# Performance work log

Measured on AMD Instinct MI355X. Metric: run time of the kernel, lower is better.

The kernel has to match this reference:

```python
import jax, jax.numpy as jnp
import numpy as np

N = 20000
E = 320000
IN_FEATS = 512
H = 4
D_HID = 256
D_OUT = 256
NEG_SLOPE = 0.2


def _gat_layer(h, src, dst, Wsrc, Wdst, al, ar, b, apply_act):
    # h: [N, Fin]; Wsrc/Wdst: [Fin, H*D]; al/ar: [H, D]; b: [H*D]
    Hh, Dd = al.shape
    fs = (h @ Wsrc).reshape(-1, Hh, Dd)  # [N, H, D] src projection
    fd = (h @ Wdst).reshape(-1, Hh, Dd)  # [N, H, D] dst projection
    el = (fs * al).sum(-1)               # [N, H]
    er = (fd * ar).sum(-1)               # [N, H]
    e = jax.nn.leaky_relu(el[src] + er[dst], NEG_SLOPE)  # [E, H]
    m = jax.lax.stop_gradient(jax.ops.segment_max(e, dst, num_segments=N))
    m = jnp.where(jnp.isfinite(m), m, 0.0)
    ex = jnp.exp(e - m[dst])
    den = jax.ops.segment_sum(ex, dst, num_segments=N)  # [N, H]
    alpha = ex / den[dst]                               # edge softmax per dst node
    msg = fs[src] * alpha[:, :, None]                   # [E, H, D]
    out = jax.ops.segment_sum(msg, dst, num_segments=N) + b.reshape(Hh, Dd)
    if apply_act:
        out = jax.nn.relu(out)
    return out  # [N, H, D]


def setup_inputs() -> dict:
    key = jax.random.key(0)
    ks = jax.random.split(key, 20)
    x = jax.random.normal(ks[0], (N, IN_FEATS), dtype=jnp.float32)
    src = jax.random.randint(ks[1], (E,), 0, N, dtype=jnp.int32)
    dst = jax.random.randint(ks[2], (E,), 0, N, dtype=jnp.int32)
    fins = [IN_FEATS, H * D_HID, H * D_HID]
    douts = [D_HID, D_HID, D_OUT]
    inp = {"x": x, "src": src, "dst": dst}
    ki = 3
    for l in range(3):
        fin, do = fins[l], douts[l]
        s = 1.0 / np.sqrt(fin)
        inp[f"Wsrc{l}"] = jax.random.normal(ks[ki], (fin, H * do), dtype=jnp.float32) * s; ki += 1
        inp[f"Wdst{l}"] = jax.random.normal(ks[ki], (fin, H * do), dtype=jnp.float32) * s; ki += 1
        inp[f"al{l}"] = jax.random.normal(ks[ki], (H, do), dtype=jnp.float32) * 0.1; ki += 1
        inp[f"ar{l}"] = jax.random.normal(ks[ki], (H, do), dtype=jnp.float32) * 0.1; ki += 1
        inp[f"b{l}"] = jnp.zeros((H * do,), dtype=jnp.float32)
    return inp


def reference(x, src, dst,
              Wsrc0, Wdst0, al0, ar0, b0,
              Wsrc1, Wdst1, al1, ar1, b1,
              Wsrc2, Wdst2, al2, ar2, b2):
    h = _gat_layer(x, src, dst, Wsrc0, Wdst0, al0, ar0, b0, True).reshape(N, -1)
    h = _gat_layer(h, src, dst, Wsrc1, Wdst1, al1, ar1, b1, True).reshape(N, -1)
    h = _gat_layer(h, src, dst, Wsrc2, Wdst2, al2, ar2, b2, False)  # [N, H, D_OUT]
    return h.mean(axis=1)  # [N, D_OUT]
```

## Files before the change

### kernel.cpp

```cpp
#include <hip/hip_runtime.h>
#include <hip/hip_bf16.h>
#include <math.h>

#define NNODES 20000
#define NPAD   20480
#define NBM    160
#define NEDGES 320000
#define HEADS  4
#define DDIM   256
#define MCOLS  1024

typedef __attribute__((ext_vector_type(8))) short short8;
typedef __attribute__((ext_vector_type(4))) float f32x4;

__device__ __forceinline__ unsigned short f2bf(float f) {
  unsigned u = __float_as_uint(f);
  unsigned r = (u + 0x7fffu + ((u >> 16) & 1u)) >> 16;
  return (unsigned short)r;
}
__device__ __forceinline__ float bf2f(unsigned short h) {
  return __uint_as_float(((unsigned)h) << 16);
}
__device__ __forceinline__ float blo(unsigned v) { return __uint_as_float(v << 16); }
__device__ __forceinline__ float bhi(unsigned v) { return __uint_as_float(v & 0xffff0000u); }

__device__ __forceinline__ void async_ld16(void* lds, const void* g) {
  __builtin_amdgcn_global_load_lds(
      (const __attribute__((address_space(1))) unsigned int*)g,
      (__attribute__((address_space(3))) unsigned int*)lds, 16, 0, 0);
}

__global__ void k_zero(int* deg, int n) {
  int i = blockIdx.x*blockDim.x + threadIdx.x;
  if (i < n) deg[i] = 0;
}
__global__ void k_hist(const int* __restrict__ dst, int* deg, int e) {
  int i = blockIdx.x*blockDim.x + threadIdx.x;
  if (i < e) atomicAdd(&deg[dst[i]], 1);
}
__global__ void k_scan(const int* __restrict__ deg, int* row_ptr, int* cursor) {
  __shared__ int sm[1024];
  int t = threadIdx.x;
  const int CH = 20;
  int base = t*CH;
  int s = 0;
  #pragma unroll
  for (int i = 0; i < CH; ++i) { int idx = base+i; if (idx < NNODES) s += deg[idx]; }
  int val = s;
  sm[t] = s; __syncthreads();
  for (int off = 1; off < 1024; off <<= 1) {
    int add = (t >= off) ? sm[t-off] : 0;
    __syncthreads();
    val += add; sm[t] = val;
    __syncthreads();
  }
  int run = val - s;
  for (int i = 0; i < CH; ++i) {
    int idx = base+i;
    if (idx < NNODES) { row_ptr[idx] = run; cursor[idx] = run; run += deg[idx]; }
  }
  if (t == 0) row_ptr[NNODES] = NEDGES;
}
__global__ void k_fill(const int* __restrict__ src, const int* __restrict__ dst,
                       int* cursor, int* srcs_sorted, int* dsts_sorted, int e) {
  int i = blockIdx.x*blockDim.x + threadIdx.x;
  if (i < e) {
    int d = dst[i];
    int pos = atomicAdd(&cursor[d], 1);
    srcs_sorted[pos] = src[i];
    dsts_sorted[pos] = d;
  }
}

__device__ __forceinline__ void fold_body(const float* __restrict__ W,
                                          const float* __restrict__ v,
                                          float* __restrict__ F, int K, int bb) {
  int wave = threadIdx.x >> 6, lane = threadIdx.x & 63;
  int p = bb*4 + wave;
  int k = p >> 2, h = p & 3;
  const float4 wv = *(const float4*)&W[(size_t)k*MCOLS + h*DDIM + lane*4];
  const float4 av = *(const float4*)&v[h*DDIM + lane*4];
  float s = wv.x*av.x + wv.y*av.y + wv.z*av.z + wv.w*av.w;
  for (int off = 32; off; off >>= 1) s += __shfl_xor(s, off);
  if (lane == 0) F[k*HEADS + h] = s;
}
__global__ __launch_bounds__(256) void k_fold_all(
    const float* Wd0, const float* ar0, float* F0,
    const float* Ws0, const float* al0, float* G0,
    const float* Wd1, const float* ar1, float* F1,
    const float* Ws1, const float* al1, float* G1,
    const float* Wd2, const float* ar2, float* F2,
    const float* Ws2, const float* al2, float* G2) {
  int b = blockIdx.x;
  if      (b < 512)  fold_body(Wd0, ar0, F0, 512,  b);
  else if (b < 1024) fold_body(Ws0, al0, G0, 512,  b - 512);
  else if (b < 2048) fold_body(Wd1, ar1, F1, 1024, b - 1024);
  else if (b < 3072) fold_body(Ws1, al1, G1, 1024, b - 2048);
  else if (b < 4096) fold_body(Wd2, ar2, F2, 1024, b - 3072);
  else               fold_body(Ws2, al2, G2, 1024, b - 4096);
}

__global__ __launch_bounds__(256) void k_prep0(
    const float* __restrict__ x, const float* __restrict__ Wal,
    const float* __restrict__ Wred,
    unsigned short* __restrict__ hi, unsigned short* __restrict__ lo,
    float* __restrict__ el, float* __restrict__ er) {
  __shared__ float red_sm[4][8];
  int n = blockIdx.x, t = threadIdx.x;
  if (n >= NNODES) {
    *(ushort2*)&hi[(size_t)n*512 + 2*t] = (ushort2){0,0};
    *(ushort2*)&lo[(size_t)n*512 + 2*t] = (ushort2){0,0};
    return;
  }
  float2 xv = *(const float2*)&x[(size_t)n*512 + 2*t];
  ushort2 h2, l2;
  h2.x = f2bf(xv.x); l2.x = f2bf(xv.x - bf2f(h2.x));
  h2.y = f2bf(xv.y); l2.y = f2bf(xv.y - bf2f(h2.y));
  *(ushort2*)&hi[(size_t)n*512 + 2*t] = h2;
  *(ushort2*)&lo[(size_t)n*512 + 2*t] = l2;
  const float4 wa0 = *(const float4*)&Wal[(2*t)*4];
  const float4 wa1 = *(const float4*)&Wal[(2*t+1)*4];
  const float4 wr0 = *(const float4*)&Wred[(2*t)*4];
  const float4 wr1 = *(const float4*)&Wred[(2*t+1)*4];
  float p[8];
  p[0] = xv.x*wa0.x + xv.y*wa1.x;
  p[1] = xv.x*wa0.y + xv.y*wa1.y;
  p[2] = xv.x*wa0.z + xv.y*wa1.z;
  p[3] = xv.x*wa0.w + xv.y*wa1.w;
  p[4] = xv.x*wr0.x + xv.y*wr1.x;
  p[5] = xv.x*wr0.y + xv.y*wr1.y;
  p[6] = xv.x*wr0.z + xv.y*wr1.z;
  p[7] = xv.x*wr0.w + xv.y*wr1.w;
  for (int off = 32; off; off >>= 1)
    #pragma unroll
    for (int j = 0; j < 8; ++j) p[j] += __shfl_xor(p[j], off);
  if ((t & 63) == 0)
    #pragma unroll
    for (int j = 0; j < 8; ++j) red_sm[t >> 6][j] = p[j];
  __syncthreads();
  if (t < 8) {
    float v = (red_sm[0][t] + red_sm[1][t]) + (red_sm[2][t] + red_sm[3][t]);
    if (t < 4) el[n*HEADS + t] = v;
    else       er[n*HEADS + (t-4)] = v;
  }
}

__global__ __launch_bounds__(256) void k_cvtw_wgt(
    const float* __restrict__ W, unsigned short* __restrict__ Th, int K,
    const float* __restrict__ el, const float* __restrict__ er,
    const int* __restrict__ srcs, const int* __restrict__ dsts,
    float* __restrict__ wb, int e4) {
  int b = blockIdx.x;
  if (b < K) {
    __shared__ float sm[32][33];
    int n0 = (b & 31)*32, k0 = (b >> 5)*32;
    int t = threadIdx.x;
    int r = t >> 3, c4 = (t & 7)*4;
    *(float4*)&sm[r][c4] = *(const float4*)&W[(size_t)(k0 + r)*MCOLS + n0 + c4];
    __syncthreads();
    ushort4 h;
    h.x = f2bf(sm[c4+0][r]);
    h.y = f2bf(sm[c4+1][r]);
    h.z = f2bf(sm[c4+2][r]);
    h.w = f2bf(sm[c4+3][r]);
    *(ushort4*)&Th[(size_t)(n0 + r)*K + k0 + c4] = h;
  } else {
    int i = (b - K)*256 + threadIdx.x;
    if (i < e4) {
      int pos = i >> 2, h = i & 3;
      float v = el[srcs[pos]*HEADS + h] + er[dsts[pos]*HEADS + h];
      v = v >= 0.f ? v : 0.2f*v;
      wb[i] = __expf(v);
    }
  }
}

template<bool SPLIT>
__global__ __launch_bounds__(256, 3) void k_gemm_mfma(
    const unsigned short* __restrict__ Ah, const unsigned short* __restrict__ Al,
    const unsigned short* __restrict__ Bh,
    unsigned short* __restrict__ Fh, int K) {
  __shared__ short sAh[128*32];
  __shared__ short sAl[SPLIT ? 128*32 : 16];
  __shared__ short sBh[128*32];
  const int t = threadIdx.x;
  const int w = t >> 6, l = t & 63;
  const int b = blockIdx.x;
  const int xcd = b & 7, kk = b >> 3;
  const int bm = xcd*20 + (kk >> 3), bn = kk & 7;
  const int m0 = (w >> 1) * 64, n0 = (w & 1) * 64;

  f32x4 acc[4][4];
  #pragma unroll
  for (int i = 0; i < 4; ++i)
    #pragma unroll
    for (int j = 0; j < 4; ++j) acc[i][j] = (f32x4){0.f, 0.f, 0.f, 0.f};

  const int srow = t >> 2, koct = (t & 3) * 8;
  const size_t r64 = (size_t)64 * K;
  const unsigned short* gAh = Ah + (size_t)(bm*128 + srow)*K + koct;
  const unsigned short* gAl = Al + (size_t)(bm*128 + srow)*K + koct;
  const unsigned short* gBh = Bh + (size_t)(bn*128 + srow)*K + koct;
  char* lAh = (char*)sAh + w*1024;
  char* lAl = (char*)sAl + w*1024;
  char* lBh = (char*)sBh + w*1024;

  const int fr = l & 15, fq = l >> 4;

  for (int k0 = 0; k0 < K; k0 += 32) {
    async_ld16(lAh,        gAh + k0);
    async_ld16(lAh + 4096, gAh + k0 + r64);
    if (SPLIT) {
      async_ld16(lAl,        gAl + k0);
      async_ld16(lAl + 4096, gAl + k0 + r64);
    }
    async_ld16(lBh,        gBh + k0);
    async_ld16(lBh + 4096, gBh + k0 + r64);
    __syncthreads();

    short8 bhv[4];
    #pragma unroll
    for (int nt = 0; nt < 4; ++nt)
      bhv[nt] = *(const short8*)&sBh[(n0 + nt*16 + fr)*32 + fq*8];
    #pragma unroll
    for (int mt = 0; mt < 4; ++mt) {
      int off = (m0 + mt*16 + fr)*32 + fq*8;
      short8 ah = *(const short8*)&sAh[off];
      #pragma unroll
      for (int nt = 0; nt < 4; ++nt)
        acc[mt][nt] = __builtin_amdgcn_mfma_f32_16x16x32_bf16(ah, bhv[nt], acc[mt][nt], 0, 0, 0);
      if (SPLIT) {
        short8 al = *(const short8*)&sAl[off];
        #pragma unroll
        for (int nt = 0; nt < 4; ++nt)
          acc[mt][nt] = __builtin_amdgcn_mfma_f32_16x16x32_bf16(al, bhv[nt], acc[mt][nt], 0, 0, 0);
      }
    }
    __syncthreads();
  }

  #pragma unroll
  for (int mt = 0; mt < 4; ++mt)
    #pragma unroll
    for (int nt = 0; nt < 4; ++nt) {
      size_t base = (size_t)(bm*128 + m0 + mt*16 + fq*4)*MCOLS + bn*128 + n0 + nt*16 + fr;
      Fh[base          ] = f2bf(acc[mt][nt][0]);
      Fh[base + MCOLS  ] = f2bf(acc[mt][nt][1]);
      Fh[base + 2*MCOLS] = f2bf(acc[mt][nt][2]);
      Fh[base + 3*MCOLS] = f2bf(acc[mt][nt][3]);
    }
}

__global__ __launch_bounds__(128) void k_agg_f(
    const unsigned short* __restrict__ fsh, const float* __restrict__ wbuf,
    const int* __restrict__ row_ptr, const int* __restrict__ srcs,
    const float* __restrict__ bias,
    const float* __restrict__ WalN, const float* __restrict__ WredN,
    unsigned short* __restrict__ Ahi,
    float* __restrict__ el_next, float* __restrict__ er_next) {
  __shared__ float red_sm[2][8];
  int n = blockIdx.x;
  int t = threadIdx.x;
  int w = t >> 6, lane = t & 63;
  int half = lane >> 5, lam = lane & 31;
  int head = w*2 + half;
  int k0 = head*DDIM + lam*8;
  if (n >= NNODES) {
    uint4 z = {0,0,0,0};
    *(uint4*)&Ahi[(size_t)n*MCOLS + k0] = z;
    return;
  }
  int beg = row_ptr[n], end = row_ptr[n+1];
  float den = 0.f;
  float ac[8];
  #pragma unroll
  for (int j = 0; j < 8; ++j) ac[j] = 0.f;
  const char* fbyte = (const char*)fsh;
  const unsigned tb = (unsigned)(k0*2);

  int nfull = (end - beg) & ~7;
  int gend = beg + nfull;
  int i = beg;
  int s[8];
  if (i < gend) {
    #pragma unroll
    for (int j = 0; j < 8; ++j) s[j] = srcs[i + j];
  }
  while (i < gend) {
    float wg[8];
    #pragma unroll
    for (int j = 0; j < 8; ++j) {
      float2 wv = *(const float2*)&wbuf[(size_t)(i + j)*HEADS + w*2];
      wg[j] = half ? wv.y : wv.x;
    }
    uint4 u[8];
    #pragma unroll
    for (int j = 0; j < 8; ++j)
      u[j] = *(const uint4*)(fbyte + ((unsigned)s[j]*2048u + tb));
    i += 8;
    if (i < gend) {
      #pragma unroll
      for (int j = 0; j < 8; ++j) s[j] = srcs[i + j];
    }
    #pragma unroll
    for (int j = 0; j < 8; ++j) {
      den += wg[j];
      ac[0] = fmaf(wg[j], blo(u[j].x), ac[0]);
      ac[1] = fmaf(wg[j], bhi(u[j].x), ac[1]);
      ac[2] = fmaf(wg[j], blo(u[j].y), ac[2]);
      ac[3] = fmaf(wg[j], bhi(u[j].y), ac[3]);
      ac[4] = fmaf(wg[j], blo(u[j].z), ac[4]);
      ac[5] = fmaf(wg[j], bhi(u[j].z), ac[5]);
      ac[6] = fmaf(wg[j], blo(u[j].w), ac[6]);
      ac[7] = fmaf(wg[j], bhi(u[j].w), ac[7]);
    }
  }
  for (; i < end; ++i) {
    int sr = srcs[i];
    float2 wv = *(const float2*)&wbuf[(size_t)i*HEADS + w*2];
    float wgt = half ? wv.y : wv.x;
    const uint4 u = *(const uint4*)(fbyte + ((unsigned)sr*2048u + tb));
    den += wgt;
    ac[0] = fmaf(wgt, blo(u.x), ac[0]);
    ac[1] = fmaf(wgt, bhi(u.x), ac[1]);
    ac[2] = fmaf(wgt, blo(u.y), ac[2]);
    ac[3] = fmaf(wgt, bhi(u.y), ac[3]);
    ac[4] = fmaf(wgt, blo(u.z), ac[4]);
    ac[5] = fmaf(wgt, bhi(u.z), ac[5]);
    ac[6] = fmaf(wgt, blo(u.w), ac[6]);
    ac[7] = fmaf(wgt, bhi(u.w), ac[7]);
  }
  float inv = den > 0.f ? 1.f/den : 0.f;
  const float4 bv0 = *(const float4*)&bias[k0];
  const float4 bv1 = *(const float4*)&bias[k0 + 4];
  float o[8];
  o[0] = fmaxf(ac[0]*inv + bv0.x, 0.f);
  o[1] = fmaxf(ac[1]*inv + bv0.y, 0.f);
  o[2] = fmaxf(ac[2]*inv + bv0.z, 0.f);
  o[3] = fmaxf(ac[3]*inv + bv0.w, 0.f);
  o[4] = fmaxf(ac[4]*inv + bv1.x, 0.f);
  o[5] = fmaxf(ac[5]*inv + bv1.y, 0.f);
  o[6] = fmaxf(ac[6]*inv + bv1.z, 0.f);
  o[7] = fmaxf(ac[7]*inv + bv1.w, 0.f);
  uint4 hp;
  hp.x = (unsigned)f2bf(o[0]) | ((unsigned)f2bf(o[1]) << 16);
  hp.y = (unsigned)f2bf(o[2]) | ((unsigned)f2bf(o[3]) << 16);
  hp.z = (unsigned)f2bf(o[4]) | ((unsigned)f2bf(o[5]) << 16);
  hp.w = (unsigned)f2bf(o[6]) | ((unsigned)f2bf(o[7]) << 16);
  *(uint4*)&Ahi[(size_t)n*MCOLS + k0] = hp;
  float p[8];
  #pragma unroll
  for (int j = 0; j < 8; ++j) p[j] = 0.f;
  #pragma unroll
  for (int j = 0; j < 8; ++j) {
    const float4 wa = *(const float4*)&WalN[(k0+j)*HEADS];
    const float4 wr = *(const float4*)&WredN[(k0+j)*HEADS];
    p[0] = fmaf(o[j], wa.x, p[0]);
    p[1] = fmaf(o[j], wa.y, p[1]);
    p[2] = fmaf(o[j], wa.z, p[2]);
    p[3] = fmaf(o[j], wa.w, p[3]);
    p[4] = fmaf(o[j], wr.x, p[4]);
    p[5] = fmaf(o[j], wr.y, p[5]);
    p[6] = fmaf(o[j], wr.z, p[6]);
    p[7] = fmaf(o[j], wr.w, p[7]);
  }
  for (int off = 32; off; off >>= 1)
    #pragma unroll
    for (int j = 0; j < 8; ++j) p[j] += __shfl_xor(p[j], off);
  if (lane == 0)
    #pragma unroll
    for (int j = 0; j < 8; ++j) red_sm[w][j] = p[j];
  __syncthreads();
  if (t < 8) {
    float v = red_sm[0][t] + red_sm[1][t];
    if (t < 4) el_next[n*HEADS + t] = v;
    else       er_next[n*HEADS + (t-4)] = v;
  }
}

__global__ __launch_bounds__(128) void k_agg_out(
    const unsigned short* __restrict__ fsh, const float* __restrict__ wbuf,
    const int* __restrict__ row_ptr, const int* __restrict__ srcs,
    const float* __restrict__ bias, float* __restrict__ out) {
  __shared__ float sm[HEADS*DDIM];
  int n = blockIdx.x;
  int t = threadIdx.x;
  int w = t >> 6, lane = t & 63;
  int half = lane >> 5, lam = lane & 31;
  int head = w*2 + half;
  int k0 = head*DDIM + lam*8;
  int beg = row_ptr[n], end = row_ptr[n+1];
  float den = 0.f;
  float ac[8];
  #pragma unroll
  for (int j = 0; j < 8; ++j) ac[j] = 0.f;
  const char* fbyte = (const char*)fsh;
  const unsigned tb = (unsigned)(k0*2);

  int nfull = (end - beg) & ~7;
  int gend = beg + nfull;
  int i = beg;
  int s[8];
  if (i < gend) {
    #pragma unroll
    for (int j = 0; j < 8; ++j) s[j] = srcs[i + j];
  }
  while (i < gend) {
    float wg[8];
    #pragma unroll
    for (int j = 0; j < 8; ++j) {
      float2 wv = *(const float2*)&wbuf[(size_t)(i + j)*HEADS + w*2];
      wg[j] = half ? wv.y : wv.x;
    }
    uint4 u[8];
    #pragma unroll
    for (int j = 0; j < 8; ++j)
      u[j] = *(const uint4*)(fbyte + ((unsigned)s[j]*2048u + tb));
    i += 8;
    if (i < gend) {
      #pragma unroll
      for (int j = 0; j < 8; ++j) s[j] = srcs[i + j];
    }
    #pragma unroll
    for (int j = 0; j < 8; ++j) {
      den += wg[j];
      ac[0] = fmaf(wg[j], blo(u[j].x), ac[0]);
      ac[1] = fmaf(wg[j], bhi(u[j].x), ac[1]);
      ac[2] = fmaf(wg[j], blo(u[j].y), ac[2]);
      ac[3] = fmaf(wg[j], bhi(u[j].y), ac[3]);
      ac[4] = fmaf(wg[j], blo(u[j].z), ac[4]);
      ac[5] = fmaf(wg[j], bhi(u[j].z), ac[5]);
      ac[6] = fmaf(wg[j], blo(u[j].w), ac[6]);
      ac[7] = fmaf(wg[j], bhi(u[j].w), ac[7]);
    }
  }
  for (; i < end; ++i) {
    int sr = srcs[i];
    float2 wv = *(const float2*)&wbuf[(size_t)i*HEADS + w*2];
    float wgt = half ? wv.y : wv.x;
    const uint4 u = *(const uint4*)(fbyte + ((unsigned)sr*2048u + tb));
    den += wgt;
    ac[0] = fmaf(wgt, blo(u.x), ac[0]);
    ac[1] = fmaf(wgt, bhi(u.x), ac[1]);
    ac[2] = fmaf(wgt, blo(u.y), ac[2]);
    ac[3] = fmaf(wgt, bhi(u.y), ac[3]);
    ac[4] = fmaf(wgt, blo(u.z), ac[4]);
    ac[5] = fmaf(wgt, bhi(u.z), ac[5]);
    ac[6] = fmaf(wgt, blo(u.w), ac[6]);
    ac[7] = fmaf(wgt, bhi(u.w), ac[7]);
  }
  float inv = den > 0.f ? 1.f/den : 0.f;
  const float4 bv0 = *(const float4*)&bias[k0];
  const float4 bv1 = *(const float4*)&bias[k0 + 4];
  sm[k0+0] = ac[0]*inv + bv0.x;
  sm[k0+1] = ac[1]*inv + bv0.y;
  sm[k0+2] = ac[2]*inv + bv0.z;
  sm[k0+3] = ac[3]*inv + bv0.w;
  sm[k0+4] = ac[4]*inv + bv1.x;
  sm[k0+5] = ac[5]*inv + bv1.y;
  sm[k0+6] = ac[6]*inv + bv1.z;
  sm[k0+7] = ac[7]*inv + bv1.w;
  __syncthreads();
  #pragma unroll
  for (int rep = 0; rep < 2; ++rep) {
    int d = t + rep*128;
    out[(size_t)n*DDIM + d] =
        0.25f*((sm[d] + sm[DDIM + d]) + (sm[2*DDIM + d] + sm[3*DDIM + d]));
  }
}

extern "C" void kernel_launch(void* const* d_in, const int* in_sizes, int n_in,
                              void* d_out, int out_size, void* d_ws, size_t ws_size,
                              hipStream_t stream) {
  const float* x   = (const float*)d_in[0];
  const int*   src = (const int*)d_in[1];
  const int*   dst = (const int*)d_in[2];
  const float* Wsrc[3] = {(const float*)d_in[3], (const float*)d_in[8],  (const float*)d_in[13]};
  const float* Wdst[3] = {(const float*)d_in[4], (const float*)d_in[9],  (const float*)d_in[14]};
  const float* al[3]   = {(const float*)d_in[5], (const float*)d_in[10], (const float*)d_in[15]};
  const float* ar[3]   = {(const float*)d_in[6], (const float*)d_in[11], (const float*)d_in[16]};
  const float* bb[3]   = {(const float*)d_in[7], (const float*)d_in[12], (const float*)d_in[17]};

  char* ws = (char*)d_ws;
  size_t off = 0;
  auto alloc = [&](size_t bytes) { void* p = ws + off; off += (bytes + 255) & ~255ull; return p; };
  unsigned short* fshB = (unsigned short*)alloc((size_t)NPAD*MCOLS*2);
  unsigned short* Ahi = (unsigned short*)alloc((size_t)NPAD*MCOLS*2);
  unsigned short* Alo = (unsigned short*)alloc((size_t)NPAD*MCOLS*2);
  unsigned short* Wth = (unsigned short*)alloc((size_t)MCOLS*MCOLS*2);
  float* elA  = (float*)alloc((size_t)NNODES*HEADS*4);
  float* elB  = (float*)alloc((size_t)NNODES*HEADS*4);
  float* erA  = (float*)alloc((size_t)NNODES*HEADS*4);
  float* erB  = (float*)alloc((size_t)NNODES*HEADS*4);
  float* wbuf = (float*)alloc((size_t)NEDGES*HEADS*4);
  float* WredB[3]; float* WalB[3];
  for (int l = 0; l < 3; ++l) {
    WredB[l] = (float*)alloc(1024*HEADS*4);
    WalB[l]  = (float*)alloc(1024*HEADS*4);
  }
  int* deg     = (int*)alloc((size_t)NNODES*4);
  int* row_ptr = (int*)alloc((size_t)(NNODES+1)*4);
  int* cursor  = (int*)alloc((size_t)NNODES*4);
  int* srcs    = (int*)alloc((size_t)NEDGES*4);
  int* dsts    = (int*)alloc((size_t)NEDGES*4);
  (void)ws_size; (void)in_sizes; (void)n_in; (void)out_size;

  k_zero<<<(NNODES+255)/256, 256, 0, stream>>>(deg, NNODES);
  k_hist<<<(NEDGES+255)/256, 256, 0, stream>>>(dst, deg, NEDGES);
  k_scan<<<1, 1024, 0, stream>>>(deg, row_ptr, cursor);
  k_fill<<<(NEDGES+255)/256, 256, 0, stream>>>(src, dst, cursor, srcs, dsts, NEDGES);

  k_fold_all<<<5120, 256, 0, stream>>>(
      Wdst[0], ar[0], WredB[0], Wsrc[0], al[0], WalB[0],
      Wdst[1], ar[1], WredB[1], Wsrc[1], al[1], WalB[1],
      Wdst[2], ar[2], WredB[2], Wsrc[2], al[2], WalB[2]);

  k_prep0<<<NPAD, 256, 0, stream>>>(x, WalB[0], WredB[0], Ahi, Alo, elA, erA);

  float* el_cur = elA; float* el_nxt = elB;
  float* er_cur = erA; float* er_nxt = erB;
  const int Fin[3] = {512, 1024, 1024};
  const int E4 = NEDGES*HEADS;
  for (int l = 0; l < 3; ++l) {
    int K = Fin[l];
    k_cvtw_wgt<<<K + (E4 + 255)/256, 256, 0, stream>>>(
        Wsrc[l], Wth, K, el_cur, er_cur, srcs, dsts, wbuf, E4);
    if (l == 0)
      k_gemm_mfma<true><<<NBM*8, 256, 0, stream>>>(Ahi, Alo, Wth, fshB, K);
    else
      k_gemm_mfma<false><<<NBM*8, 256, 0, stream>>>(Ahi, Alo, Wth, fshB, K);
    if (l < 2) {
      k_agg_f<<<NPAD, 128, 0, stream>>>(fshB, wbuf, row_ptr, srcs, bb[l],
                                        WalB[l+1], WredB[l+1], Ahi, el_nxt, er_nxt);
      float* t1 = el_cur; el_cur = el_nxt; el_nxt = t1;
      float* t2 = er_cur; er_cur = er_nxt; er_nxt = t2;
    } else {
      k_agg_out<<<NNODES, 128, 0, stream>>>(fshB, wbuf, row_ptr, srcs, bb[l],
                                            (float*)d_out);
    }
  }
}
```

Before: 732.5 us.

## Split aggregation into per-slice blocks with two-phase source-range gather for L2 locality

Aggregation kernels now give each block one of 8 feature slices of 128 channels and several nodes per wave. Each wave's 4 lane groups gather edges in parallel, and each gather runs two passes over halves of the source-node range so the gathered rows stay within a smaller working set in cache. Edge weights are stored head-major so per-head reads are contiguous. Partial el/er projections are summed with atomics into buffers zeroed by memsets, and the final layer writes per-head partials that a new combine kernel averages. In exchange, every edge list is read twice, and the code adds atomics, extra launches and cross-lane shuffle reductions.

```diff
diff --git a/kernel.cpp b/kernel.cpp
--- a/kernel.cpp
+++ b/kernel.cpp
@@ -167,7 +167,8 @@
   } else {
     int i = (b - K)*256 + threadIdx.x;
     if (i < e4) {
-      int pos = i >> 2, h = i & 3;
+      int h = i / NEDGES;
+      int pos = i - h*NEDGES;
       float v = el[srcs[pos]*HEADS + h] + er[dsts[pos]*HEADS + h];
       v = v >= 0.f ? v : 0.2f*v;
       wb[i] = __expf(v);
@@ -251,222 +252,190 @@
     }
 }
 
-__global__ __launch_bounds__(128) void k_agg_f(
+__device__ __forceinline__ void slice_gather(
+    const char* __restrict__ fb, const float* __restrict__ wbh,
+    const int* __restrict__ srcs, int beg, int end, unsigned soff, int g,
+    float* ac, float& den) {
+  #pragma unroll
+  for (int ph = 0; ph < 2; ++ph) {
+    const int lo = ph * (NNODES/2);
+    const int hi = lo + (NNODES/2);
+    int e = beg + g;
+    int sr0 = 0; float wg0 = 0.f;
+    if (e < end) {
+      int sr = srcs[e];
+      float wv = wbh[e];
+      bool inr = (sr >= lo) & (sr < hi);
+      sr0 = inr ? sr : 0;
+      wg0 = inr ? wv : 0.f;
+    }
+    for (int i = beg; i < end; i += 4) {
+      const uint4 u = *(const uint4*)(fb + ((unsigned)sr0*2048u + soff));
+      int e2 = i + 4 + g;
+      int sr1 = 0; float wg1 = 0.f;
+      if (e2 < end) {
+        int sr = srcs[e2];
+        float wv = wbh[e2];
+        bool inr = (sr >= lo) & (sr < hi);
+        sr1 = inr ? sr : 0;
+        wg1 = inr ? wv : 0.f;
+      }
+      den += wg0;
+      ac[0] = fmaf(wg0, blo(u.x), ac[0]);
+      ac[1] = fmaf(wg0, bhi(u.x), ac[1]);
+      ac[2] = fmaf(wg0, blo(u.y), ac[2]);
+      ac[3] = fmaf(wg0, bhi(u.y), ac[3]);
+      ac[4] = fmaf(wg0, blo(u.z), ac[4]);
+      ac[5] = fmaf(wg0, bhi(u.z), ac[5]);
+      ac[6] = fmaf(wg0, blo(u.w), ac[6]);
+      ac[7] = fmaf(wg0, bhi(u.w), ac[7]);
+      sr0 = sr1; wg0 = wg1;
+    }
+  }
+}
+
+__global__ __launch_bounds__(256) void k_agg_f(
     const unsigned short* __restrict__ fsh, const float* __restrict__ wbuf,
     const int* __restrict__ row_ptr, const int* __restrict__ srcs,
     const float* __restrict__ bias,
     const float* __restrict__ WalN, const float* __restrict__ WredN,
     unsigned short* __restrict__ Ahi,
     float* __restrict__ el_next, float* __restrict__ er_next) {
-  __shared__ float red_sm[2][8];
-  int n = blockIdx.x;
-  int t = threadIdx.x;
-  int w = t >> 6, lane = t & 63;
-  int half = lane >> 5, lam = lane & 31;
-  int head = w*2 + half;
-  int k0 = head*DDIM + lam*8;
-  if (n >= NNODES) {
-    uint4 z = {0,0,0,0};
-    *(uint4*)&Ahi[(size_t)n*MCOLS + k0] = z;
-    return;
-  }
-  int beg = row_ptr[n], end = row_ptr[n+1];
-  float den = 0.f;
-  float ac[8];
-  #pragma unroll
-  for (int j = 0; j < 8; ++j) ac[j] = 0.f;
-  const char* fbyte = (const char*)fsh;
-  const unsigned tb = (unsigned)(k0*2);
-
-  int nfull = (end - beg) & ~7;
-  int gend = beg + nfull;
-  int i = beg;
-  int s[8];
-  if (i < gend) {
-    #pragma unroll
-    for (int j = 0; j < 8; ++j) s[j] = srcs[i + j];
-  }
-  while (i < gend) {
-    float wg[8];
+  const int b = blockIdx.x;
+  const int s = b & 7;
+  const int gb = b >> 3;
+  const int t = threadIdx.x;
+  const int wv = t >> 6, lane = t & 63;
+  const int g = lane >> 4, sl = lane & 15;
+  const int head = s >> 1, half = s & 1;
+  const int k0 = head*DDIM + half*128 + sl*8;
+  const unsigned soff = (unsigned)(s*256 + sl*16);
+  const char* fb = (const char*)fsh;
+  const float* wbh = wbuf + (size_t)head*NEDGES;
+
+  const int nbase = gb*20 + wv*5;
+  for (int nn = 0; nn < 5; ++nn) {
+    const int n = nbase + nn;
+    if (n >= NNODES) {
+      if (lane < 16) {
+        uint4 z = {0,0,0,0};
+        *(uint4*)&Ahi[(size_t)n*MCOLS + k0] = z;
+      }
+      continue;
+    }
+    const int beg = row_ptr[n], end = row_ptr[n+1];
+    float den = 0.f;
+    float ac[8] = {0.f,0.f,0.f,0.f,0.f,0.f,0.f,0.f};
+    slice_gather(fb, wbh, srcs, beg, end, soff, g, ac, den);
     #pragma unroll
     for (int j = 0; j < 8; ++j) {
-      float2 wv = *(const float2*)&wbuf[(size_t)(i + j)*HEADS + w*2];
-      wg[j] = half ? wv.y : wv.x;
-    }
-    uint4 u[8];
-    #pragma unroll
-    for (int j = 0; j < 8; ++j)
-      u[j] = *(const uint4*)(fbyte + ((unsigned)s[j]*2048u + tb));
-    i += 8;
-    if (i < gend) {
+      ac[j] += __shfl_xor(ac[j], 16);
+      ac[j] += __shfl_xor(ac[j], 32);
+    }
+    den += __shfl_xor(den, 16);
+    den += __shfl_xor(den, 32);
+    const float inv = den > 0.f ? 1.f/den : 0.f;
+    const float4 bv0 = *(const float4*)&bias[k0];
+    const float4 bv1 = *(const float4*)&bias[k0 + 4];
+    float o[8];
+    o[0] = fmaxf(ac[0]*inv + bv0.x, 0.f);
+    o[1] = fmaxf(ac[1]*inv + bv0.y, 0.f);
+    o[2] = fmaxf(ac[2]*inv + bv0.z, 0.f);
+    o[3] = fmaxf(ac[3]*inv + bv0.w, 0.f);
+    o[4] = fmaxf(ac[4]*inv + bv1.x, 0.f);
+    o[5] = fmaxf(ac[5]*inv + bv1.y, 0.f);
+    o[6] = fmaxf(ac[6]*inv + bv1.z, 0.f);
+    o[7] = fmaxf(ac[7]*inv + bv1.w, 0.f);
+    if (lane < 16) {
+      uint4 hp;
+      hp.x = (unsigned)f2bf(o[0]) | ((unsigned)f2bf(o[1]) << 16);
+      hp.y = (unsigned)f2bf(o[2]) | ((unsigned)f2bf(o[3]) << 16);
+      hp.z = (unsigned)f2bf(o[4]) | ((unsigned)f2bf(o[5]) << 16);
+      hp.w = (unsigned)f2bf(o[6]) | ((unsigned)f2bf(o[7]) << 16);
+      *(uint4*)&Ahi[(size_t)n*MCOLS + k0] = hp;
+    }
+    float p[8] = {0.f,0.f,0.f,0.f,0.f,0.f,0.f,0.f};
+    #pragma unroll
+    for (int j = 0; j < 8; ++j) {
+      const float4 wa = *(const float4*)&WalN[(k0+j)*HEADS];
+      const float4 wr = *(const float4*)&WredN[(k0+j)*HEADS];
+      p[0] = fmaf(o[j], wa.x, p[0]);
+      p[1] = fmaf(o[j], wa.y, p[1]);
+      p[2] = fmaf(o[j], wa.z, p[2]);
+      p[3] = fmaf(o[j], wa.w, p[3]);
+      p[4] = fmaf(o[j], wr.x, p[4]);
+      p[5] = fmaf(o[j], wr.y, p[5]);
+      p[6] = fmaf(o[j], wr.z, p[6]);
+      p[7] = fmaf(o[j], wr.w, p[7]);
+    }
+    #pragma unroll
+    for (int off2 = 1; off2 < 16; off2 <<= 1)
       #pragma unroll
-      for (int j = 0; j < 8; ++j) s[j] = srcs[i + j];
-    }
-    #pragma unroll
-    for (int j = 0; j < 8; ++j) {
-      den += wg[j];
-      ac[0] = fmaf(wg[j], blo(u[j].x), ac[0]);
-      ac[1] = fmaf(wg[j], bhi(u[j].x), ac[1]);
-      ac[2] = fmaf(wg[j], blo(u[j].y), ac[2]);
-      ac[3] = fmaf(wg[j], bhi(u[j].y), ac[3]);
-      ac[4] = fmaf(wg[j], blo(u[j].z), ac[4]);
-      ac[5] = fmaf(wg[j], bhi(u[j].z), ac[5]);
-      ac[6] = fmaf(wg[j], blo(u[j].w), ac[6]);
-      ac[7] = fmaf(wg[j], bhi(u[j].w), ac[7]);
-    }
-  }
-  for (; i < end; ++i) {
-    int sr = srcs[i];
-    float2 wv = *(const float2*)&wbuf[(size_t)i*HEADS + w*2];
-    float wgt = half ? wv.y : wv.x;
-    const uint4 u = *(const uint4*)(fbyte + ((unsigned)sr*2048u + tb));
-    den += wgt;
-    ac[0] = fmaf(wgt, blo(u.x), ac[0]);
-    ac[1] = fmaf(wgt, bhi(u.x), ac[1]);
-    ac[2] = fmaf(wgt, blo(u.y), ac[2]);
-    ac[3] = fmaf(wgt, bhi(u.y), ac[3]);
-    ac[4] = fmaf(wgt, blo(u.z), ac[4]);
-    ac[5] = fmaf(wgt, bhi(u.z), ac[5]);
-    ac[6] = fmaf(wgt, blo(u.w), ac[6]);
-    ac[7] = fmaf(wgt, bhi(u.w), ac[7]);
-  }
-  float inv = den > 0.f ? 1.f/den : 0.f;
-  const float4 bv0 = *(const float4*)&bias[k0];
-  const float4 bv1 = *(const float4*)&bias[k0 + 4];
-  float o[8];
-  o[0] = fmaxf(ac[0]*inv + bv0.x, 0.f);
-  o[1] = fmaxf(ac[1]*inv + bv0.y, 0.f);
-  o[2] = fmaxf(ac[2]*inv + bv0.z, 0.f);
-  o[3] = fmaxf(ac[3]*inv + bv0.w, 0.f);
-  o[4] = fmaxf(ac[4]*inv + bv1.x, 0.f);
-  o[5] = fmaxf(ac[5]*inv + bv1.y, 0.f);
-  o[6] = fmaxf(ac[6]*inv + bv1.z, 0.f);
-  o[7] = fmaxf(ac[7]*inv + bv1.w, 0.f);
-  uint4 hp;
-  hp.x = (unsigned)f2bf(o[0]) | ((unsigned)f2bf(o[1]) << 16);
-  hp.y = (unsigned)f2bf(o[2]) | ((unsigned)f2bf(o[3]) << 16);
-  hp.z = (unsigned)f2bf(o[4]) | ((unsigned)f2bf(o[5]) << 16);
-  hp.w = (unsigned)f2bf(o[6]) | ((unsigned)f2bf(o[7]) << 16);
-  *(uint4*)&Ahi[(size_t)n*MCOLS + k0] = hp;
-  float p[8];
-  #pragma unroll
-  for (int j = 0; j < 8; ++j) p[j] = 0.f;
-  #pragma unroll
-  for (int j = 0; j < 8; ++j) {
-    const float4 wa = *(const float4*)&WalN[(k0+j)*HEADS];
-    const float4 wr = *(const float4*)&WredN[(k0+j)*HEADS];
-    p[0] = fmaf(o[j], wa.x, p[0]);
-    p[1] = fmaf(o[j], wa.y, p[1]);
-    p[2] = fmaf(o[j], wa.z, p[2]);
-    p[3] = fmaf(o[j], wa.w, p[3]);
-    p[4] = fmaf(o[j], wr.x, p[4]);
-    p[5] = fmaf(o[j], wr.y, p[5]);
-    p[6] = fmaf(o[j], wr.z, p[6]);
-    p[7] = fmaf(o[j], wr.w, p[7]);
-  }
-  for (int off = 32; off; off >>= 1)
-    #pragma unroll
-    for (int j = 0; j < 8; ++j) p[j] += __shfl_xor(p[j], off);
-  if (lane == 0)
-    #pragma unroll
-    for (int j = 0; j < 8; ++j) red_sm[w][j] = p[j];
-  __syncthreads();
-  if (t < 8) {
-    float v = red_sm[0][t] + red_sm[1][t];
-    if (t < 4) el_next[n*HEADS + t] = v;
-    else       er_next[n*HEADS + (t-4)] = v;
-  }
-}
-
-__global__ __launch_bounds__(128) void k_agg_out(
+      for (int j = 0; j < 8; ++j) p[j] += __shfl_xor(p[j], off2);
+    if (lane == 0) {
+      #pragma unroll
+      for (int j = 0; j < 4; ++j) atomicAdd(&el_next[n*HEADS + j], p[j]);
+      #pragma unroll
+      for (int j = 0; j < 4; ++j) atomicAdd(&er_next[n*HEADS + j], p[4+j]);
+    }
+  }
+}
+
+__global__ __launch_bounds__(256) void k_agg_out(
     const unsigned short* __restrict__ fsh, const float* __restrict__ wbuf,
     const int* __restrict__ row_ptr, const int* __restrict__ srcs,
-    const float* __restrict__ bias, float* __restrict__ out) {
-  __shared__ float sm[HEADS*DDIM];
-  int n = blockIdx.x;
-  int t = threadIdx.x;
-  int w = t >> 6, lane = t & 63;
-  int half = lane >> 5, lam = lane & 31;
-  int head = w*2 + half;
-  int k0 = head*DDIM + lam*8;
-  int beg = row_ptr[n], end = row_ptr[n+1];
-  float den = 0.f;
-  float ac[8];
-  #pragma unroll
-  for (int j = 0; j < 8; ++j) ac[j] = 0.f;
-  const char* fbyte = (const char*)fsh;
-  const unsigned tb = (unsigned)(k0*2);
-
-  int nfull = (end - beg) & ~7;
-  int gend = beg + nfull;
-  int i = beg;
-  int s[8];
-  if (i < gend) {
-    #pragma unroll
-    for (int j = 0; j < 8; ++j) s[j] = srcs[i + j];
-  }
-  while (i < gend) {
-    float wg[8];
+    const float* __restrict__ bias, float* __restrict__ opart) {
+  const int b = blockIdx.x;
+  const int s = b & 7;
+  const int gb = b >> 3;
+  const int t = threadIdx.x;
+  const int wv = t >> 6, lane = t & 63;
+  const int g = lane >> 4, sl = lane & 15;
+  const int head = s >> 1, half = s & 1;
+  const int k0 = head*DDIM + half*128 + sl*8;
+  const unsigned soff = (unsigned)(s*256 + sl*16);
+  const char* fb = (const char*)fsh;
+  const float* wbh = wbuf + (size_t)head*NEDGES;
+
+  const int nbase = gb*20 + wv*5;
+  for (int nn = 0; nn < 5; ++nn) {
+    const int n = nbase + nn;
+    const int beg = row_ptr[n], end = row_ptr[n+1];
+    float den = 0.f;
+    float ac[8] = {0.f,0.f,0.f,0.f,0.f,0.f,0.f,0.f};
+    slice_gather(fb, wbh, srcs, beg, end, soff, g, ac, den);
     #pragma unroll
     for (int j = 0; j < 8; ++j) {
-      float2 wv = *(const float2*)&wbuf[(size_t)(i + j)*HEADS + w*2];
-      wg[j] = half ? wv.y : wv.x;
-    }
-    uint4 u[8];
-    #pragma unroll
-    for (int j = 0; j < 8; ++j)
-      u[j] = *(const uint4*)(fbyte + ((unsigned)s[j]*2048u + tb));
-    i += 8;
-    if (i < gend) {
-      #pragma unroll
-      for (int j = 0; j < 8; ++j) s[j] = srcs[i + j];
-    }
-    #pragma unroll
-    for (int j = 0; j < 8; ++j) {
-      den += wg[j];
-      ac[0] = fmaf(wg[j], blo(u[j].x), ac[0]);
-      ac[1] = fmaf(wg[j], bhi(u[j].x), ac[1]);
-      ac[2] = fmaf(wg[j], blo(u[j].y), ac[2]);
-      ac[3] = fmaf(wg[j], bhi(u[j].y), ac[3]);
-      ac[4] = fmaf(wg[j], blo(u[j].z), ac[4]);
-      ac[5] = fmaf(wg[j], bhi(u[j].z), ac[5]);
-      ac[6] = fmaf(wg[j], blo(u[j].w), ac[6]);
-      ac[7] = fmaf(wg[j], bhi(u[j].w), ac[7]);
-    }
-  }
-  for (; i < end; ++i) {
-    int sr = srcs[i];
-    float2 wv = *(const float2*)&wbuf[(size_t)i*HEADS + w*2];
-    float wgt = half ? wv.y : wv.x;
-    const uint4 u = *(const uint4*)(fbyte + ((unsigned)sr*2048u + tb));
-    den += wgt;
-    ac[0] = fmaf(wgt, blo(u.x), ac[0]);
-    ac[1] = fmaf(wgt, bhi(u.x), ac[1]);
-    ac[2] = fmaf(wgt, blo(u.y), ac[2]);
-    ac[3] = fmaf(wgt, bhi(u.y), ac[3]);
-    ac[4] = fmaf(wgt, blo(u.z), ac[4]);
-    ac[5] = fmaf(wgt, bhi(u.z), ac[5]);
-    ac[6] = fmaf(wgt, blo(u.w), ac[6]);
-    ac[7] = fmaf(wgt, bhi(u.w), ac[7]);
-  }
-  float inv = den > 0.f ? 1.f/den : 0.f;
-  const float4 bv0 = *(const float4*)&bias[k0];
-  const float4 bv1 = *(const float4*)&bias[k0 + 4];
-  sm[k0+0] = ac[0]*inv + bv0.x;
-  sm[k0+1] = ac[1]*inv + bv0.y;
-  sm[k0+2] = ac[2]*inv + bv0.z;
-  sm[k0+3] = ac[3]*inv + bv0.w;
-  sm[k0+4] = ac[4]*inv + bv1.x;
-  sm[k0+5] = ac[5]*inv + bv1.y;
-  sm[k0+6] = ac[6]*inv + bv1.z;
-  sm[k0+7] = ac[7]*inv + bv1.w;
-  __syncthreads();
-  #pragma unroll
-  for (int rep = 0; rep < 2; ++rep) {
-    int d = t + rep*128;
-    out[(size_t)n*DDIM + d] =
-        0.25f*((sm[d] + sm[DDIM + d]) + (sm[2*DDIM + d] + sm[3*DDIM + d]));
-  }
+      ac[j] += __shfl_xor(ac[j], 16);
+      ac[j] += __shfl_xor(ac[j], 32);
+    }
+    den += __shfl_xor(den, 16);
+    den += __shfl_xor(den, 32);
+    const float inv = den > 0.f ? 1.f/den : 0.f;
+    const float4 bv0 = *(const float4*)&bias[k0];
+    const float4 bv1 = *(const float4*)&bias[k0 + 4];
+    if (lane < 16) {
+      float4 v0, v1;
+      v0.x = ac[0]*inv + bv0.x;
+      v0.y = ac[1]*inv + bv0.y;
+      v0.z = ac[2]*inv + bv0.z;
+      v0.w = ac[3]*inv + bv0.w;
+      v1.x = ac[4]*inv + bv1.x;
+      v1.y = ac[5]*inv + bv1.y;
+      v1.z = ac[6]*inv + bv1.z;
+      v1.w = ac[7]*inv + bv1.w;
+      size_t ob = (size_t)head*NNODES*DDIM + (size_t)n*DDIM + half*128 + sl*8;
+      *(float4*)&opart[ob]     = v0;
+      *(float4*)&opart[ob + 4] = v1;
+    }
+  }
+}
+
+__global__ __launch_bounds__(256) void k_combine(
+    const float* __restrict__ opart, float* __restrict__ out) {
+  const size_t i = (size_t)blockIdx.x*256 + threadIdx.x;
+  const size_t NH = (size_t)NNODES*DDIM;
+  out[i] = 0.25f*((opart[i] + opart[i + NH]) + (opart[i + 2*NH] + opart[i + 3*NH]));
 }
 
 extern "C" void kernel_launch(void* const* d_in, const int* in_sizes, int n_in,
@@ -504,6 +473,7 @@
   int* srcs    = (int*)alloc((size_t)NEDGES*4);
   int* dsts    = (int*)alloc((size_t)NEDGES*4);
   (void)ws_size; (void)in_sizes; (void)n_in; (void)out_size;
+  float* opart = (float*)Ahi;
 
   k_zero<<<(NNODES+255)/256, 256, 0, stream>>>(deg, NNODES);
   k_hist<<<(NEDGES+255)/256, 256, 0, stream>>>(dst, deg, NEDGES);
@@ -530,13 +500,16 @@
     else
       k_gemm_mfma<false><<<NBM*8, 256, 0, stream>>>(Ahi, Alo, Wth, fshB, K);
     if (l < 2) {
-      k_agg_f<<<NPAD, 128, 0, stream>>>(fshB, wbuf, row_ptr, srcs, bb[l],
-                                        WalB[l+1], WredB[l+1], Ahi, el_nxt, er_nxt);
+      hipMemsetAsync(el_nxt, 0, (size_t)NNODES*HEADS*4, stream);
+      hipMemsetAsync(er_nxt, 0, (size_t)NNODES*HEADS*4, stream);
+      k_agg_f<<<1024*8, 256, 0, stream>>>(fshB, wbuf, row_ptr, srcs, bb[l],
+                                          WalB[l+1], WredB[l+1], Ahi, el_nxt, er_nxt);
       float* t1 = el_cur; el_cur = el_nxt; el_nxt = t1;
       float* t2 = er_cur; er_cur = er_nxt; er_nxt = t2;
     } else {
-      k_agg_out<<<NNODES, 128, 0, stream>>>(fshB, wbuf, row_ptr, srcs, bb[l],
-                                            (float*)d_out);
-    }
-  }
-}
+      k_agg_out<<<1000*8, 256, 0, stream>>>(fshB, wbuf, row_ptr, srcs, bb[l],
+                                            opart);
+      k_combine<<<(NNODES*DDIM)/256, 256, 0, stream>>>(opart, (float*)d_out);
+    }
+  }
+}
```

New measurement: 1.361 ms. +85.8%, slower.

## Aggregate raw inputs before projection in layer 0 and drop split-bf16 GEMM

Applied to the files above, without the earlier changes.

For the first layer, the order of operations is changed: per-head softmax-weighted aggregation of the 512-wide bf16 input features happens first, into a 2048-wide per-head buffer, and the projection GEMM runs afterwards with a block-diagonal A operand and fused bias+ReLU epilogue. A separate kernel then computes el/er for layer 1 from the GEMM output. The hi/lo split-precision path for x is removed, so the layer-0 GEMM does a single bf16 MFMA pass. The aim is to gather narrower rows during aggregation and halve the MFMA work in layer 0, at the cost of lower input precision and an extra el/er kernel.

```diff
diff --git a/kernel.cpp b/kernel.cpp
--- a/kernel.cpp
+++ b/kernel.cpp
@@ -103,21 +103,19 @@
 __global__ __launch_bounds__(256) void k_prep0(
     const float* __restrict__ x, const float* __restrict__ Wal,
     const float* __restrict__ Wred,
-    unsigned short* __restrict__ hi, unsigned short* __restrict__ lo,
+    unsigned short* __restrict__ xh,
     float* __restrict__ el, float* __restrict__ er) {
   __shared__ float red_sm[4][8];
   int n = blockIdx.x, t = threadIdx.x;
   if (n >= NNODES) {
-    *(ushort2*)&hi[(size_t)n*512 + 2*t] = (ushort2){0,0};
-    *(ushort2*)&lo[(size_t)n*512 + 2*t] = (ushort2){0,0};
+    *(ushort2*)&xh[(size_t)n*512 + 2*t] = (ushort2){0,0};
     return;
   }
   float2 xv = *(const float2*)&x[(size_t)n*512 + 2*t];
-  ushort2 h2, l2;
-  h2.x = f2bf(xv.x); l2.x = f2bf(xv.x - bf2f(h2.x));
-  h2.y = f2bf(xv.y); l2.y = f2bf(xv.y - bf2f(h2.y));
-  *(ushort2*)&hi[(size_t)n*512 + 2*t] = h2;
-  *(ushort2*)&lo[(size_t)n*512 + 2*t] = l2;
+  ushort2 h2;
+  h2.x = f2bf(xv.x);
+  h2.y = f2bf(xv.y);
+  *(ushort2*)&xh[(size_t)n*512 + 2*t] = h2;
   const float4 wa0 = *(const float4*)&Wal[(2*t)*4];
   const float4 wa1 = *(const float4*)&Wal[(2*t+1)*4];
   const float4 wr0 = *(const float4*)&Wred[(2*t)*4];
@@ -131,6 +129,42 @@
   p[5] = xv.x*wr0.y + xv.y*wr1.y;
   p[6] = xv.x*wr0.z + xv.y*wr1.z;
   p[7] = xv.x*wr0.w + xv.y*wr1.w;
+  for (int off = 32; off; off >>= 1)
+    #pragma unroll
+    for (int j = 0; j < 8; ++j) p[j] += __shfl_xor(p[j], off);
+  if ((t & 63) == 0)
+    #pragma unroll
+    for (int j = 0; j < 8; ++j) red_sm[t >> 6][j] = p[j];
+  __syncthreads();
+  if (t < 8) {
+    float v = (red_sm[0][t] + red_sm[1][t]) + (red_sm[2][t] + red_sm[3][t]);
+    if (t < 4) el[n*HEADS + t] = v;
+    else       er[n*HEADS + (t-4)] = v;
+  }
+}
+
+__global__ __launch_bounds__(256) void k_elr(
+    const unsigned short* __restrict__ h, const float* __restrict__ Wal,
+    const float* __restrict__ Wred,
+    float* __restrict__ el, float* __restrict__ er) {
+  __shared__ float red_sm[4][8];
+  int n = blockIdx.x, t = threadIdx.x;
+  ushort4 hv = *(const ushort4*)&h[(size_t)n*MCOLS + 4*t];
+  float xv[4] = {bf2f(hv.x), bf2f(hv.y), bf2f(hv.z), bf2f(hv.w)};
+  float p[8] = {0.f,0.f,0.f,0.f,0.f,0.f,0.f,0.f};
+  #pragma unroll
+  for (int j = 0; j < 4; ++j) {
+    const float4 wa = *(const float4*)&Wal[(4*t + j)*HEADS];
+    const float4 wr = *(const float4*)&Wred[(4*t + j)*HEADS];
+    p[0] = fmaf(xv[j], wa.x, p[0]);
+    p[1] = fmaf(xv[j], wa.y, p[1]);
+    p[2] = fmaf(xv[j], wa.z, p[2]);
+    p[3] = fmaf(xv[j], wa.w, p[3]);
+    p[4] = fmaf(xv[j], wr.x, p[4]);
+    p[5] = fmaf(xv[j], wr.y, p[5]);
+    p[6] = fmaf(xv[j], wr.z, p[6]);
+    p[7] = fmaf(xv[j], wr.w, p[7]);
+  }
   for (int off = 32; off; off >>= 1)
     #pragma unroll
     for (int j = 0; j < 8; ++j) p[j] += __shfl_xor(p[j], off);
@@ -175,13 +209,111 @@
   }
 }
 
-template<bool SPLIT>
-__global__ __launch_bounds__(256, 3) void k_gemm_mfma(
-    const unsigned short* __restrict__ Ah, const unsigned short* __restrict__ Al,
-    const unsigned short* __restrict__ Bh,
-    unsigned short* __restrict__ Fh, int K) {
+__global__ __launch_bounds__(128) void k_agg5(
+    const unsigned short* __restrict__ xh, const float* __restrict__ wbuf,
+    const int* __restrict__ row_ptr, const int* __restrict__ srcs,
+    unsigned short* __restrict__ g) {
+  int t = threadIdx.x, w = t >> 6, lane = t & 63;
+  int n = blockIdx.x*2 + w;
+  const unsigned tb = (unsigned)(lane*16);
+  if (n >= NNODES) {
+    uint4 z = {0,0,0,0};
+    #pragma unroll
+    for (int h = 0; h < 4; ++h)
+      *(uint4*)&g[(size_t)n*2048 + h*512 + lane*8] = z;
+    return;
+  }
+  int beg = row_ptr[n], end = row_ptr[n+1];
+  float den0 = 0.f, den1 = 0.f, den2 = 0.f, den3 = 0.f;
+  float a0[8] = {0,0,0,0,0,0,0,0};
+  float a1[8] = {0,0,0,0,0,0,0,0};
+  float a2[8] = {0,0,0,0,0,0,0,0};
+  float a3[8] = {0,0,0,0,0,0,0,0};
+  const char* fb = (const char*)xh;
+
+  int nfull = (end - beg) & ~3;
+  int gend = beg + nfull;
+  int i = beg;
+  int s[4];
+  if (i < gend) {
+    #pragma unroll
+    for (int j = 0; j < 4; ++j) s[j] = srcs[i + j];
+  }
+  while (i < gend) {
+    float4 wv[4];
+    #pragma unroll
+    for (int j = 0; j < 4; ++j) wv[j] = *(const float4*)&wbuf[(size_t)(i + j)*4];
+    uint4 u[4];
+    #pragma unroll
+    for (int j = 0; j < 4; ++j)
+      u[j] = *(const uint4*)(fb + ((unsigned)s[j]*1024u + tb));
+    i += 4;
+    if (i < gend) {
+      #pragma unroll
+      for (int j = 0; j < 4; ++j) s[j] = srcs[i + j];
+    }
+    #pragma unroll
+    for (int j = 0; j < 4; ++j) {
+      den0 += wv[j].x; den1 += wv[j].y; den2 += wv[j].z; den3 += wv[j].w;
+      float xv[8] = {blo(u[j].x), bhi(u[j].x), blo(u[j].y), bhi(u[j].y),
+                     blo(u[j].z), bhi(u[j].z), blo(u[j].w), bhi(u[j].w)};
+      #pragma unroll
+      for (int d = 0; d < 8; ++d) {
+        a0[d] = fmaf(wv[j].x, xv[d], a0[d]);
+        a1[d] = fmaf(wv[j].y, xv[d], a1[d]);
+        a2[d] = fmaf(wv[j].z, xv[d], a2[d]);
+        a3[d] = fmaf(wv[j].w, xv[d], a3[d]);
+      }
+    }
+  }
+  for (; i < end; ++i) {
+    int sr = srcs[i];
+    float4 wv = *(const float4*)&wbuf[(size_t)i*4];
+    const uint4 u = *(const uint4*)(fb + ((unsigned)sr*1024u + tb));
+    den0 += wv.x; den1 += wv.y; den2 += wv.z; den3 += wv.w;
+    float xv[8] = {blo(u.x), bhi(u.x), blo(u.y), bhi(u.y),
+                   blo(u.z), bhi(u.z), blo(u.w), bhi(u.w)};
+    #pragma unroll
+    for (int d = 0; d < 8; ++d) {
+      a0[d] = fmaf(wv.x, xv[d], a0[d]);
+      a1[d] = fmaf(wv.y, xv[d], a1[d]);
+      a2[d] = fmaf(wv.z, xv[d], a2[d]);
+      a3[d] = fmaf(wv.w, xv[d], a3[d]);
+    }
+  }
+  float i0 = den0 > 0.f ? 1.f/den0 : 0.f;
+  float i1 = den1 > 0.f ? 1.f/den1 : 0.f;
+  float i2 = den2 > 0.f ? 1.f/den2 : 0.f;
+  float i3 = den3 > 0.f ? 1.f/den3 : 0.f;
+  uint4 p;
+  p.x = (unsigned)f2bf(a0[0]*i0) | ((unsigned)f2bf(a0[1]*i0) << 16);
+  p.y = (unsigned)f2bf(a0[2]*i0) | ((unsigned)f2bf(a0[3]*i0) << 16);
+  p.z = (unsigned)f2bf(a0[4]*i0) | ((unsigned)f2bf(a0[5]*i0) << 16);
+  p.w = (unsigned)f2bf(a0[6]*i0) | ((unsigned)f2bf(a0[7]*i0) << 16);
+  *(uint4*)&g[(size_t)n*2048 + 0*512 + lane*8] = p;
+  p.x = (unsigned)f2bf(a1[0]*i1) | ((unsigned)f2bf(a1[1]*i1) << 16);
+  p.y = (unsigned)f2bf(a1[2]*i1) | ((unsigned)f2bf(a1[3]*i1) << 16);
+  p.z = (unsigned)f2bf(a1[4]*i1) | ((unsigned)f2bf(a1[5]*i1) << 16);
+  p.w = (unsigned)f2bf(a1[6]*i1) | ((unsigned)f2bf(a1[7]*i1) << 16);
+  *(uint4*)&g[(size_t)n*2048 + 1*512 + lane*8] = p;
+  p.x = (unsigned)f2bf(a2[0]*i2) | ((unsigned)f2bf(a2[1]*i2) << 16);
+  p.y = (unsigned)f2bf(a2[2]*i2) | ((unsigned)f2bf(a2[3]*i2) << 16);
+  p.z = (unsigned)f2bf(a2[4]*i2) | ((unsigned)f2bf(a2[5]*i2) << 16);
+  p.w = (unsigned)f2bf(a2[6]*i2) | ((unsigned)f2bf(a2[7]*i2) << 16);
+  *(uint4*)&g[(size_t)n*2048 + 2*512 + lane*8] = p;
+  p.x = (unsigned)f2bf(a3[0]*i3) | ((unsigned)f2bf(a3[1]*i3) << 16);
+  p.y = (unsigned)f2bf(a3[2]*i3) | ((unsigned)f2bf(a3[3]*i3) << 16);
+  p.z = (unsigned)f2bf(a3[4]*i3) | ((unsigned)f2bf(a3[5]*i3) << 16);
+  p.w = (unsigned)f2bf(a3[6]*i3) | ((unsigned)f2bf(a3[7]*i3) << 16);
+  *(uint4*)&g[(size_t)n*2048 + 3*512 + lane*8] = p;
+}
+
+template<int BD, int EPI>
+__global__ __launch_bounds__(256, 3) void k_gemm(
+    const unsigned short* __restrict__ A, const unsigned short* __restrict__ B,
+    const float* __restrict__ bias, unsigned short* __restrict__ Fh,
+    int K, int lda) {
   __shared__ short sAh[128*32];
-  __shared__ short sAl[SPLIT ? 128*32 : 16];
   __shared__ short sBh[128*32];
   const int t = threadIdx.x;
   const int w = t >> 6, l = t & 63;
@@ -197,25 +329,21 @@
     for (int j = 0; j < 4; ++j) acc[i][j] = (f32x4){0.f, 0.f, 0.f, 0.f};
 
   const int srow = t >> 2, koct = (t & 3) * 8;
-  const size_t r64 = (size_t)64 * K;
-  const unsigned short* gAh = Ah + (size_t)(bm*128 + srow)*K + koct;
-  const unsigned short* gAl = Al + (size_t)(bm*128 + srow)*K + koct;
-  const unsigned short* gBh = Bh + (size_t)(bn*128 + srow)*K + koct;
-  char* lAh = (char*)sAh + w*1024;
-  char* lAl = (char*)sAl + w*1024;
-  char* lBh = (char*)sBh + w*1024;
+  const size_t rA64 = (size_t)64 * lda;
+  const size_t rB64 = (size_t)64 * K;
+  const unsigned short* gA = A + (size_t)(bm*128 + srow)*lda
+                               + (BD ? (bn >> 1)*512 : 0) + koct;
+  const unsigned short* gB = B + (size_t)(bn*128 + srow)*K + koct;
+  char* lA = (char*)sAh + w*1024;
+  char* lB = (char*)sBh + w*1024;
 
   const int fr = l & 15, fq = l >> 4;
 
   for (int k0 = 0; k0 < K; k0 += 32) {
-    async_ld16(lAh,        gAh + k0);
-    async_ld16(lAh + 4096, gAh + k0 + r64);
-    if (SPLIT) {
-      async_ld16(lAl,        gAl + k0);
-      async_ld16(lAl + 4096, gAl + k0 + r64);
-    }
-    async_ld16(lBh,        gBh + k0);
-    async_ld16(lBh + 4096, gBh + k0 + r64);
+    async_ld16(lA,        gA + k0);
+    async_ld16(lA + 4096, gA + k0 + rA64);
+    async_ld16(lB,        gB + k0);
+    async_ld16(lB + 4096, gB + k0 + rB64);
     __syncthreads();
 
     short8 bhv[4];
@@ -229,26 +357,30 @@
       #pragma unroll
       for (int nt = 0; nt < 4; ++nt)
         acc[mt][nt] = __builtin_amdgcn_mfma_f32_16x16x32_bf16(ah, bhv[nt], acc[mt][nt], 0, 0, 0);
-      if (SPLIT) {
-        short8 al = *(const short8*)&sAl[off];
-        #pragma unroll
-        for (int nt = 0; nt < 4; ++nt)
-          acc[mt][nt] = __builtin_amdgcn_mfma_f32_16x16x32_bf16(al, bhv[nt], acc[mt][nt], 0, 0, 0);
+    }
+    __syncthreads();
+  }
+
+  #pragma unroll
+  for (int nt = 0; nt < 4; ++nt) {
+    const int col = bn*128 + n0 + nt*16 + fr;
+    float bv = (EPI == 1) ? bias[col] : 0.f;
+    #pragma unroll
+    for (int mt = 0; mt < 4; ++mt) {
+      size_t base = (size_t)(bm*128 + m0 + mt*16 + fq*4)*MCOLS + col;
+      if (EPI == 1) {
+        Fh[base          ] = f2bf(fmaxf(acc[mt][nt][0] + bv, 0.f));
+        Fh[base + MCOLS  ] = f2bf(fmaxf(acc[mt][nt][1] + bv, 0.f));
+        Fh[base + 2*MCOLS] = f2bf(fmaxf(acc[mt][nt][2] + bv, 0.f));
+        Fh[base + 3*MCOLS] = f2bf(fmaxf(acc[mt][nt][3] + bv, 0.f));
+      } else {
+        Fh[base          ] = f2bf(acc[mt][nt][0]);
+        Fh[base + MCOLS  ] = f2bf(acc[mt][nt][1]);
+        Fh[base + 2*MCOLS] = f2bf(acc[mt][nt][2]);
+        Fh[base + 3*MCOLS] = f2bf(acc[mt][nt][3]);
       }
     }
-    __syncthreads();
-  }
-
-  #pragma unroll
-  for (int mt = 0; mt < 4; ++mt)
-    #pragma unroll
-    for (int nt = 0; nt < 4; ++nt) {
-      size_t base = (size_t)(bm*128 + m0 + mt*16 + fq*4)*MCOLS + bn*128 + n0 + nt*16 + fr;
-      Fh[base          ] = f2bf(acc[mt][nt][0]);
-      Fh[base + MCOLS  ] = f2bf(acc[mt][nt][1]);
-      Fh[base + 2*MCOLS] = f2bf(acc[mt][nt][2]);
-      Fh[base + 3*MCOLS] = f2bf(acc[mt][nt][3]);
-    }
+  }
 }
 
 __global__ __launch_bounds__(128) void k_agg_f(
@@ -484,10 +616,11 @@
   char* ws = (char*)d_ws;
   size_t off = 0;
   auto alloc = [&](size_t bytes) { void* p = ws + off; off += (bytes + 255) & ~255ull; return p; };
+  unsigned short* xh   = (unsigned short*)alloc((size_t)NPAD*512*2);
+  unsigned short* gbuf = (unsigned short*)alloc((size_t)NPAD*2048*2);
+  unsigned short* hbuf = (unsigned short*)alloc((size_t)NPAD*MCOLS*2);
   unsigned short* fshB = (unsigned short*)alloc((size_t)NPAD*MCOLS*2);
-  unsigned short* Ahi = (unsigned short*)alloc((size_t)NPAD*MCOLS*2);
-  unsigned short* Alo = (unsigned short*)alloc((size_t)NPAD*MCOLS*2);
-  unsigned short* Wth = (unsigned short*)alloc((size_t)MCOLS*MCOLS*2);
+  unsigned short* Wth  = (unsigned short*)alloc((size_t)MCOLS*MCOLS*2);
   float* elA  = (float*)alloc((size_t)NNODES*HEADS*4);
   float* elB  = (float*)alloc((size_t)NNODES*HEADS*4);
   float* erA  = (float*)alloc((size_t)NNODES*HEADS*4);
@@ -515,28 +648,25 @@
       Wdst[1], ar[1], WredB[1], Wsrc[1], al[1], WalB[1],
       Wdst[2], ar[2], WredB[2], Wsrc[2], al[2], WalB[2]);
 
-  k_prep0<<<NPAD, 256, 0, stream>>>(x, WalB[0], WredB[0], Ahi, Alo, elA, erA);
-
-  float* el_cur = elA; float* el_nxt = elB;
-  float* er_cur = erA; float* er_nxt = erB;
-  const int Fin[3] = {512, 1024, 1024};
+  k_prep0<<<NPAD, 256, 0, stream>>>(x, WalB[0], WredB[0], xh, elA, erA);
+
   const int E4 = NEDGES*HEADS;
-  for (int l = 0; l < 3; ++l) {
-    int K = Fin[l];
-    k_cvtw_wgt<<<K + (E4 + 255)/256, 256, 0, stream>>>(
-        Wsrc[l], Wth, K, el_cur, er_cur, srcs, dsts, wbuf, E4);
-    if (l == 0)
-      k_gemm_mfma<true><<<NBM*8, 256, 0, stream>>>(Ahi, Alo, Wth, fshB, K);
-    else
-      k_gemm_mfma<false><<<NBM*8, 256, 0, stream>>>(Ahi, Alo, Wth, fshB, K);
-    if (l < 2) {
-      k_agg_f<<<NPAD, 128, 0, stream>>>(fshB, wbuf, row_ptr, srcs, bb[l],
-                                        WalB[l+1], WredB[l+1], Ahi, el_nxt, er_nxt);
-      float* t1 = el_cur; el_cur = el_nxt; el_nxt = t1;
-      float* t2 = er_cur; er_cur = er_nxt; er_nxt = t2;
-    } else {
-      k_agg_out<<<NNODES, 128, 0, stream>>>(fshB, wbuf, row_ptr, srcs, bb[l],
-                                            (float*)d_out);
-    }
-  }
-}
+
+  k_cvtw_wgt<<<512 + (E4 + 255)/256, 256, 0, stream>>>(
+      Wsrc[0], Wth, 512, elA, erA, srcs, dsts, wbuf, E4);
+  k_agg5<<<NPAD/2, 128, 0, stream>>>(xh, wbuf, row_ptr, srcs, gbuf);
+  k_gemm<1, 1><<<NBM*8, 256, 0, stream>>>(gbuf, Wth, bb[0], hbuf, 512, 2048);
+  k_elr<<<NNODES, 256, 0, stream>>>(hbuf, WalB[1], WredB[1], elB, erB);
+
+  k_cvtw_wgt<<<1024 + (E4 + 255)/256, 256, 0, stream>>>(
+      Wsrc[1], Wth, 1024, elB, erB, srcs, dsts, wbuf, E4);
+  k_gemm<0, 0><<<NBM*8, 256, 0, stream>>>(hbuf, Wth, nullptr, fshB, 1024, 1024);
+  k_agg_f<<<NPAD, 128, 0, stream>>>(fshB, wbuf, row_ptr, srcs, bb[1],
+                                    WalB[2], WredB[2], hbuf, elA, erA);
+
+  k_cvtw_wgt<<<1024 + (E4 + 255)/256, 256, 0, stream>>>(
+      Wsrc[2], Wth, 1024, elA, erA, srcs, dsts, wbuf, E4);
+  k_gemm<0, 0><<<NBM*8, 256, 0, stream>>>(hbuf, Wth, nullptr, fshB, 1024, 1024);
+  k_agg_out<<<NNODES, 128, 0, stream>>>(fshB, wbuf, row_ptr, srcs, bb[2],
+                                        (float*)d_out);
+}
```

Result: faster. 705.6 us (-3.7%).
